# Kernel optimization log

Measured on AMD Instinct MI355X. Metric: run time of the kernel, lower is better.

Reference implementation:

```python
import jax, jax.numpy as jnp
import numpy as np

HEADS = 16


def setup_inputs() -> dict:
    key = jax.random.key(0)
    k1, k2, k3 = jax.random.split(key, 3)
    B, N, C = 4, 2048, 1024
    x = jax.random.normal(k1, (B, N, C), dtype=jnp.float32)
    w_qkv = jax.random.normal(k2, (C, 3 * C), dtype=jnp.float32) * (C ** -0.5)
    b_qkv = jnp.zeros((3 * C,), dtype=jnp.float32)
    w_out = jax.random.normal(k3, (C, C), dtype=jnp.float32) * (C ** -0.5)
    b_out = jnp.zeros((C,), dtype=jnp.float32)
    return {"x": x, "w_qkv": w_qkv, "b_qkv": b_qkv, "w_out": w_out, "b_out": b_out}


def reference(x, w_qkv, b_qkv, w_out, b_out):
    # Dropout layers act as identity in eval mode.
    B, N, C = x.shape
    H = HEADS
    Dh = C // H
    scale = Dh ** -0.5
    qkv = x @ w_qkv + b_qkv                        # [B, N, 3C]
    qkv = qkv.reshape(B, N, 3, H, Dh)
    q = qkv[:, :, 0].transpose(0, 2, 1, 3)         # [B, H, N, Dh]
    k = qkv[:, :, 1].transpose(0, 2, 1, 3)
    v = qkv[:, :, 2].transpose(0, 2, 1, 3)
    attn = jnp.einsum('bhnd,bhmd->bhnm', q, k) * scale
    attn = jax.nn.softmax(attn, axis=-1)
    out = jnp.einsum('bhnm,bhmd->bhnd', attn, v)   # [B, H, N, Dh]
    out = out.transpose(0, 2, 1, 3).reshape(B, N, C)
    return out @ w_out + b_out
```

## Files before the change

kernel.cpp:

```cpp
#include <hip/hip_runtime.h>

typedef __attribute__((ext_vector_type(8))) short bf16x8;
typedef __attribute__((ext_vector_type(4))) float f32x4;
typedef __attribute__((ext_vector_type(16))) float f32x16;

__device__ __forceinline__ ushort f2bf(float f) {
  union { float f; unsigned u; } v; v.f = f;
  unsigned r = v.u + 0x7fffu + ((v.u >> 16) & 1u);
  return (ushort)(r >> 16);
}

__device__ __forceinline__ float bf2f(ushort u) {
  union { float f; unsigned u; } v; v.u = (unsigned)u << 16;
  return v.f;
}

__device__ __forceinline__ unsigned cvt_pk_bf16(float lo, float hi) {
  unsigned r;
  asm("v_cvt_pk_bf16_f32 %0, %1, %2" : "=v"(r) : "v"(lo), "v"(hi));
  return r;
}

__device__ __forceinline__ void permlane32_swap(unsigned& x, unsigned& y) {
  asm("v_permlane32_swap_b32 %0, %1" : "+v"(x), "+v"(y));
}

__device__ __forceinline__ void gload_lds16(const void* g, void* l) {
  __builtin_amdgcn_global_load_lds(
      (const __attribute__((address_space(1))) void*)g,
      (__attribute__((address_space(3))) void*)l, 16, 0, 0);
}


__global__ void cvt_f32_bf16(const float* __restrict__ s, ushort* __restrict__ d, int n) {
  int i = (blockIdx.x * blockDim.x + threadIdx.x) * 4;
  int stride = gridDim.x * blockDim.x * 4;
  for (; i < n; i += stride) {
    float4 v = *reinterpret_cast<const float4*>(s + i);
    ushort4 o;
    o.x = f2bf(v.x); o.y = f2bf(v.y); o.z = f2bf(v.z); o.w = f2bf(v.w);
    *reinterpret_cast<ushort4*>(d + i) = o;
  }
}

__global__ void transpose_cvt(const float* __restrict__ src, ushort* __restrict__ dst,
                              int R, int C) {
  __shared__ float tile[32][33];
  int c0 = blockIdx.x * 32, r0 = blockIdx.y * 32;
  int tx = threadIdx.x, ty = threadIdx.y;
  #pragma unroll
  for (int i = 0; i < 32; i += 8)
    tile[ty + i][tx] = src[(size_t)(r0 + ty + i) * C + c0 + tx];
  __syncthreads();
  #pragma unroll
  for (int i = 0; i < 32; i += 8)
    dst[(size_t)(c0 + ty + i) * R + r0 + tx] = f2bf(tile[tx][ty + i]);
}


#define QK_STAGE(Sp, Gp, base, kt)                                             \
  {                                                                            \
    _Pragma("unroll")                                                          \
    for (int c_ = 0; c_ < 4; ++c_) {                                           \
      const int qq_ = c_ * 512 + tid;                                          \
      const int row_ = qq_ >> 3;                                               \
      const int so_ = ((qq_ & 7) ^ (row_ & 7)) * 8;                            \
      gload_lds16(Gp + (size_t)((base) + row_) * 1024 + (kt) + so_,            \
                  (char*)Sp + qq_ * 16);                                       \
    }                                                                          \
  }

#define QK_LDA(buf, mh)                                                        \
  {                                                                            \
    _Pragma("unroll")                                                          \
    for (int mi = 0; mi < 4; ++mi) {                                           \
      const int row_ = wm * 128 + (mh) * 64 + mi * 16 + lr;                    \
      const char* p_ = (const char*)&sA[buf][0] + row_ * 128;                  \
      const int sw_ = (row_ & 7) << 4;                                         \
      af[mi][0] = *(const bf16x8*)(p_ + ((lg * 16) ^ sw_));                    \
      af[mi][1] = *(const bf16x8*)(p_ + ((64 + lg * 16) ^ sw_));               \
    }                                                                          \
  }

#define QK_LDB(buf, nh)                                                        \
  {                                                                            \
    _Pragma("unroll")                                                          \
    for (int ni = 0; ni < 2; ++ni) {                                           \
      const int row_ = wn * 64 + (nh) * 32 + ni * 16 + lr;                     \
      const char* p_ = (const char*)&sB[buf][0] + row_ * 128;                  \
      const int sw_ = (row_ & 7) << 4;                                         \
      bf[ni][0] = *(const bf16x8*)(p_ + ((lg * 16) ^ sw_));                    \
      bf[ni][1] = *(const bf16x8*)(p_ + ((64 + lg * 16) ^ sw_));               \
    }                                                                          \
  }

#define QK_MMQ(mh, nh)                                                         \
  {                                                                            \
    _Pragma("unroll")                                                          \
    for (int kk = 0; kk < 2; ++kk)                                             \
      _Pragma("unroll")                                                        \
      for (int mi = 0; mi < 4; ++mi)                                           \
        _Pragma("unroll")                                                      \
        for (int ni = 0; ni < 2; ++ni)                                         \
          acc[mh][mi][nh][ni] = __builtin_amdgcn_mfma_f32_16x16x32_bf16(       \
              af[mi][kk], bf[ni][kk], acc[mh][mi][nh][ni], 0, 0, 0);           \
  }

#define QK_SYNC_MMQ(mh, nh)                                                    \
  __builtin_amdgcn_s_barrier();                                                \
  asm volatile("s_waitcnt lgkmcnt(0)" ::: "memory");                           \
  __builtin_amdgcn_sched_barrier(0);                                           \
  __builtin_amdgcn_s_setprio(1);                                               \
  QK_MMQ(mh, nh);                                                              \
  __builtin_amdgcn_s_setprio(0);                                               \
  __builtin_amdgcn_s_barrier();

__global__ __launch_bounds__(512, 1) void gemm_qk(const ushort* __restrict__ A,
                                                  const ushort* __restrict__ Bt,
                                                  const float* __restrict__ bias,
                                                  ushort* __restrict__ q,
                                                  ushort* __restrict__ k) {
  __shared__ __align__(16) ushort sA[2][256 * 64];
  __shared__ __align__(16) ushort sB[2][256 * 64];
  const int tid = threadIdx.x, lane = tid & 63, w = tid >> 6;
  const int wm = w >> 2, wn = w & 3;
  const int lr = lane & 15, lg = lane >> 4;

  const int id = blockIdx.x;
  const int xcd = id & 7, j = id >> 3;
  const int by = xcd * 4 + (j & 3);
  const int bx = j >> 2;
  const int bm = by * 256, bn = bx * 256;

  f32x4 acc[2][4][2][2] = {};
  bf16x8 af[4][2], bf[2][2];

  QK_STAGE(&sA[0][0], A, bm, 0);
  QK_STAGE(&sB[0][0], Bt, bn, 0);
  asm volatile("s_waitcnt vmcnt(0)" ::: "memory");
  __builtin_amdgcn_s_barrier();

  for (int T = 0; T < 16; ++T) {
    const int cur = T & 1;
    const bool pf = (T + 1 < 16);
    QK_LDA(cur, 0); QK_LDB(cur, 0);
    if (pf) QK_STAGE(&sA[cur ^ 1][0], A, bm, (T + 1) * 64);
    QK_SYNC_MMQ(0, 0);
    QK_LDB(cur, 1);
    if (pf) QK_STAGE(&sB[cur ^ 1][0], Bt, bn, (T + 1) * 64);
    QK_SYNC_MMQ(0, 1);
    QK_LDA(cur, 1);
    QK_SYNC_MMQ(1, 1);
    QK_LDB(cur, 0);
    asm volatile("s_waitcnt vmcnt(0)" ::: "memory");
    QK_SYNC_MMQ(1, 0);
  }

  ushort* const dst = (bn < 1024) ? q : k;
  const int cb = bn & 1023;
  #pragma unroll
  for (int mh = 0; mh < 2; ++mh)
    #pragma unroll
    for (int mi = 0; mi < 4; ++mi)
      #pragma unroll
      for (int nh = 0; nh < 2; ++nh)
        #pragma unroll
        for (int ni = 0; ni < 2; ++ni) {
          const int cq = cb + wn * 64 + nh * 32 + ni * 16 + lr;
          const int h = cq >> 6, d = cq & 63;
          const float bb = bias[bn + wn * 64 + nh * 32 + ni * 16 + lr];
          #pragma unroll
          for (int r = 0; r < 4; ++r) {
            const int row = bm + wm * 128 + mh * 64 + mi * 16 + lg * 4 + r;
            const int b_ = row >> 11, n = row & 2047;
            const int bh = b_ * 16 + h;
            dst[((size_t)bh * 2048 + n) * 64 + d] = f2bf(acc[mh][mi][nh][ni][r] + bb);
          }
        }
}


#define GEMM_STAGE(buf, Ap, Bp, kt)                                            \
  {                                                                            \
    _Pragma("unroll")                                                          \
    for (int c_ = 0; c_ < 4; ++c_) {                                           \
      const int qq_ = c_ * 256 + tid;                                          \
      const int row_ = qq_ >> 3;                                               \
      const int so_ = ((qq_ & 7) ^ (row_ & 7)) * 8;                            \
      gload_lds16(Ap + (size_t)(bm + row_) * 1024 + (kt) + so_,                \
                  (char*)sA + (buf) * 16384 + qq_ * 16);                       \
      gload_lds16(Bp + (size_t)(bn + row_) * 1024 + (kt) + so_,                \
                  (char*)sB + (buf) * 16384 + qq_ * 16);                       \
    }                                                                          \
  }

#define GEMM_COMPUTE(buf)                                                      \
  {                                                                            \
    const char* bA_ = (const char*)sA + (buf) * 16384;                         \
    const char* bB_ = (const char*)sB + (buf) * 16384;                         \
    bf16x8 af[4][2], bfr[4][2];                                                \
    _Pragma("unroll")                                                          \
    for (int mi = 0; mi < 4; ++mi) {                                           \
      const int row_ = wr * 64 + mi * 16 + lr;                                 \
      const char* p_ = bA_ + row_ * 128;                                       \
      const int sw_ = (row_ & 7) << 4;                                         \
      af[mi][0] = *(const bf16x8*)(p_ + ((lg * 16) ^ sw_));                    \
      af[mi][1] = *(const bf16x8*)(p_ + ((64 + lg * 16) ^ sw_));               \
    }                                                                          \
    _Pragma("unroll")                                                          \
    for (int ni = 0; ni < 4; ++ni) {                                           \
      const int row_ = wc * 64 + ni * 16 + lr;                                 \
      const char* p_ = bB_ + row_ * 128;                                       \
      const int sw_ = (row_ & 7) << 4;                                         \
      bfr[ni][0] = *(const bf16x8*)(p_ + ((lg * 16) ^ sw_));                   \
      bfr[ni][1] = *(const bf16x8*)(p_ + ((64 + lg * 16) ^ sw_));              \
    }                                                                          \
    _Pragma("unroll")                                                          \
    for (int kk = 0; kk < 2; ++kk)                                             \
      _Pragma("unroll")                                                        \
      for (int mi = 0; mi < 4; ++mi)                                           \
        _Pragma("unroll")                                                      \
        for (int ni = 0; ni < 4; ++ni)                                         \
          acc[mi][ni] = __builtin_amdgcn_mfma_f32_16x16x32_bf16(               \
              af[mi][kk], bfr[ni][kk], acc[mi][ni], 0, 0, 0);                  \
  }

#define GEMM_PIPELINE(Ap, Bp)                                                  \
  GEMM_STAGE(0, Ap, Bp, 0);                                                    \
  for (int T = 0; T < 16; ++T) {                                               \
    if (T + 1 < 16) {                                                          \
      GEMM_STAGE((T + 1) & 1, Ap, Bp, (T + 1) * 64);                           \
      asm volatile("s_waitcnt vmcnt(8)" ::: "memory");                         \
    } else {                                                                   \
      asm volatile("s_waitcnt vmcnt(0)" ::: "memory");                         \
    }                                                                          \
    __builtin_amdgcn_s_barrier();                                              \
    __builtin_amdgcn_sched_barrier(0);                                         \
    GEMM_COMPUTE(T & 1);                                                       \
    __builtin_amdgcn_s_barrier();                                              \
  }

#define GEMM_PROLOG                                                            \
  __shared__ __align__(16) ushort sA[2][128 * 64];                             \
  __shared__ __align__(16) ushort sB[2][128 * 64];                             \
  const int tid = threadIdx.x;                                                 \
  const int lane = tid & 63;                                                   \
  const int w = tid >> 6;                                                      \
  const int wr = w >> 1, wc = w & 1;                                           \
  const int lr = lane & 15, lg = lane >> 4;                                    \
  f32x4 acc[4][4] = {};


__global__ __launch_bounds__(256) void gemm_vT(const ushort* __restrict__ A,
                                               const ushort* __restrict__ Bt,
                                               const float* __restrict__ bias,
                                               ushort* __restrict__ vT) {
  GEMM_PROLOG;
  const int id = blockIdx.x;
  const int xcd = id & 7, j = id >> 3;
  const int bnb = xcd * 8 + (j & 7);
  const int bmb = j >> 3;
  const int bm = bmb * 128;
  const int bn = bnb * 128;

  GEMM_PIPELINE(A, Bt);

  const int b_ = bn >> 11, n0 = bn & 2047;
  #pragma unroll
  for (int mi = 0; mi < 4; ++mi)
    #pragma unroll
    for (int ni = 0; ni < 4; ++ni) {
      const int ncol = wc * 64 + ni * 16 + lr;
      #pragma unroll
      for (int r = 0; r < 4; ++r) {
        const int m = wr * 64 + mi * 16 + lg * 4 + r;
        const int vc = bm + m;
        const int h = vc >> 6, d = vc & 63;
        const int bh = b_ * 16 + h;
        const float bb = bias[vc];
        vT[((size_t)bh * 64 + d) * 2048 + n0 + ncol] = f2bf(acc[mi][ni][r] + bb);
      }
    }
}


__global__ __launch_bounds__(256) void gemm_out(const ushort* __restrict__ A,
                                                const ushort* __restrict__ Bt,
                                                const float* __restrict__ bias,
                                                float* __restrict__ out) {
  GEMM_PROLOG;
  const int id = blockIdx.x;
  const int xcd = id & 7, j = id >> 3;
  const int by = xcd * 8 + (j & 7);
  const int bx = j >> 3;
  const int bm = by * 128;
  const int bn = bx * 128;

  GEMM_PIPELINE(A, Bt);

  #pragma unroll
  for (int mi = 0; mi < 4; ++mi)
    #pragma unroll
    for (int ni = 0; ni < 4; ++ni) {
      const int col = bn + wc * 64 + ni * 16 + lr;
      const float bb = bias[col];
      #pragma unroll
      for (int r = 0; r < 4; ++r) {
        const int row = bm + wr * 64 + mi * 16 + lg * 4 + r;
        out[(size_t)row * 1024 + col] = acc[mi][ni][r] + bb;
      }
    }
}


__global__ __launch_bounds__(512, 2) void attn_fwd(const ushort* __restrict__ q,
                                                   const ushort* __restrict__ k,
                                                   const ushort* __restrict__ vT,
                                                   ushort* __restrict__ o) {
  __shared__ __align__(16) ushort sK[2][64 * 64];
  __shared__ __align__(16) ushort sV[2][64 * 64];

  const int tid = threadIdx.x, lane = tid & 63, w = tid >> 6;
  const int id = blockIdx.x;
  const int xcd = id & 7, j = id >> 3;
  const int bh = xcd * 8 + (j & 7);
  const int qx = j >> 3;
  const int qrow0 = qx * 256 + w * 32;

  const ushort* Qb = q + (size_t)bh * 2048 * 64;
  const ushort* Kb = k + (size_t)bh * 2048 * 64;
  const ushort* Vb = vT + (size_t)bh * 64 * 2048;
  const int lq = lane & 31, hi = lane >> 5;

  const int srow = lane >> 3;
  const int ssw = ((lane & 7) ^ srow) * 8;
  const int krow = w * 8 + srow;

  gload_lds16(Kb + (size_t)krow * 64 + ssw, &sK[0][w * 512]);
  gload_lds16(Vb + (size_t)krow * 2048 + 0 + ssw, &sV[0][w * 512]);

  const float qs = 0.125f * 1.44269504f;
  bf16x8 qf[4];
  #pragma unroll
  for (int dk = 0; dk < 4; ++dk) {
    bf16x8 t = *(const bf16x8*)(Qb + (size_t)(qrow0 + lq) * 64 + dk * 16 + hi * 8);
    #pragma unroll
    for (int jj = 0; jj < 8; ++jj)
      t[jj] = (short)f2bf(bf2f((ushort)t[jj]) * qs);
    qf[dk] = t;
  }

  float m_run = -1e30f, l_run = 0.f;
  f32x16 oacc[2] = {};

  for (int t = 0; t < 32; ++t) {
    const int cur = t & 1;
    if (t + 1 < 32) {
      const int kv2 = (t + 1) << 6;
      gload_lds16(Kb + (size_t)(kv2 + krow) * 64 + ssw, &sK[cur ^ 1][w * 512]);
      gload_lds16(Vb + (size_t)krow * 2048 + kv2 + ssw, &sV[cur ^ 1][w * 512]);
      asm volatile("s_waitcnt vmcnt(2)" ::: "memory");
    } else {
      asm volatile("s_waitcnt vmcnt(0)" ::: "memory");
    }
    __builtin_amdgcn_s_barrier();
    __builtin_amdgcn_sched_barrier(0);

    const char* kb_ = (const char*)&sK[cur][0];
    const char* vb_ = (const char*)&sV[cur][0];

    f32x16 S[2] = {};
    __builtin_amdgcn_s_setprio(1);
    #pragma unroll
    for (int kvt = 0; kvt < 2; ++kvt) {
      const int row = kvt * 32 + lq;
      const int rsw = (row & 7) << 4;
      #pragma unroll
      for (int dk = 0; dk < 4; ++dk) {
        bf16x8 kf = *(const bf16x8*)(kb_ + row * 128 + ((dk * 32 + hi * 16) ^ rsw));
        S[kvt] = __builtin_amdgcn_mfma_f32_32x32x16_bf16(kf, qf[dk], S[kvt], 0, 0, 0);
      }
    }
    __builtin_amdgcn_s_setprio(0);

    float mx = S[0][0];
    #pragma unroll
    for (int kvt = 0; kvt < 2; ++kvt)
      #pragma unroll
      for (int r = 0; r < 16; ++r) mx = fmaxf(mx, S[kvt][r]);
    const float rm = fmaxf(mx, __shfl_xor(mx, 32, 64));

    if (!__all(rm <= m_run + 8.f)) {
      const float mnew = fmaxf(m_run, rm);
      const float corr = __builtin_amdgcn_exp2f(m_run - mnew);
      m_run = mnew;
      l_run *= corr;
      float cq[16];
      #pragma unroll
      for (int r = 0; r < 16; ++r)
        cq[r] = __shfl(corr, (r & 3) + 8 * (r >> 2) + 4 * hi, 64);
      #pragma unroll
      for (int dt = 0; dt < 2; ++dt)
        #pragma unroll
        for (int r = 0; r < 16; ++r) oacc[dt][r] *= cq[r];
    }

    float psum = 0.f;
    unsigned pk_[2][8];
    #pragma unroll
    for (int kvt = 0; kvt < 2; ++kvt) {
      float e[16];
      #pragma unroll
      for (int r = 0; r < 16; ++r) {
        e[r] = __builtin_amdgcn_exp2f(S[kvt][r] - m_run);
        psum += e[r];
      }
      #pragma unroll
      for (int g = 0; g < 4; ++g) {
        pk_[kvt][g * 2 + 0] = cvt_pk_bf16(e[4 * g + 0], e[4 * g + 1]);
        pk_[kvt][g * 2 + 1] = cvt_pk_bf16(e[4 * g + 2], e[4 * g + 3]);
      }
    }
    psum += __shfl_xor(psum, 32, 64);
    l_run += psum;

    __builtin_amdgcn_s_setprio(1);
    #pragma unroll
    for (int kvt = 0; kvt < 2; ++kvt)
      #pragma unroll
      for (int cc = 0; cc < 2; ++cc) {
        unsigned x0 = pk_[kvt][4 * cc + 0], x1 = pk_[kvt][4 * cc + 1];
        unsigned y0 = pk_[kvt][4 * cc + 2], y1 = pk_[kvt][4 * cc + 3];
        permlane32_swap(x0, y0);
        permlane32_swap(x1, y1);
        union { unsigned u[4]; bf16x8 v; } Am;
        Am.u[0] = x0; Am.u[1] = x1; Am.u[2] = y0; Am.u[3] = y1;
        const int cg = kvt * 2 + cc;
        #pragma unroll
        for (int dt = 0; dt < 2; ++dt) {
          const int row = dt * 32 + lq;
          bf16x8 vf = *(const bf16x8*)(vb_ + row * 128 + ((cg * 32 + hi * 16) ^ ((row & 7) << 4)));
          oacc[dt] = __builtin_amdgcn_mfma_f32_32x32x16_bf16(Am.v, vf, oacc[dt], 0, 0, 0);
        }
      }
    __builtin_amdgcn_s_setprio(0);
    __builtin_amdgcn_s_barrier();
  }

  const int b_ = bh >> 4, h = bh & 15;
  float lf[16];
  #pragma unroll
  for (int r = 0; r < 16; ++r)
    lf[r] = __builtin_amdgcn_rcpf(__shfl(l_run, (r & 3) + 8 * (r >> 2) + 4 * hi, 64));
  #pragma unroll
  for (int dt = 0; dt < 2; ++dt)
    #pragma unroll
    for (int r = 0; r < 16; ++r) {
      const int n = qrow0 + (r & 3) + 8 * (r >> 2) + 4 * hi;
      o[(((size_t)b_ * 2048 + n) * 16 + h) * 64 + dt * 32 + lq] = f2bf(oacc[dt][r] * lf[r]);
    }
}


extern "C" void kernel_launch(void* const* d_in, const int* in_sizes, int n_in,
                              void* d_out, int out_size, void* d_ws, size_t ws_size,
                              hipStream_t stream) {
  const float* x = (const float*)d_in[0];
  const float* w_qkv = (const float*)d_in[1];
  const float* b_qkv = (const float*)d_in[2];
  const float* w_out = (const float*)d_in[3];
  const float* b_out = (const float*)d_in[4];
  float* out = (float*)d_out;
  char* ws = (char*)d_ws;

  ushort* xb    = (ushort*)(ws);
  ushort* wqkvT = (ushort*)(ws + 16777216);
  ushort* woutT = (ushort*)(ws + 23068672);
  ushort* qb    = (ushort*)(ws + 25165824);
  ushort* kb    = (ushort*)(ws + 41943040);
  ushort* vTb   = (ushort*)(ws + 58720256);
  ushort* attnb = (ushort*)(ws + 75497472);

  cvt_f32_bf16<<<2048, 256, 0, stream>>>(x, xb, 8192 * 1024);
  transpose_cvt<<<dim3(96, 32), dim3(32, 8), 0, stream>>>(w_qkv, wqkvT, 1024, 3072);
  transpose_cvt<<<dim3(32, 32), dim3(32, 8), 0, stream>>>(w_out, woutT, 1024, 1024);
  gemm_qk<<<256, 512, 0, stream>>>(xb, wqkvT, b_qkv, qb, kb);
  gemm_vT<<<512, 256, 0, stream>>>(wqkvT + 2048 * 1024, xb, b_qkv + 2048, vTb);
  attn_fwd<<<512, 512, 0, stream>>>(qb, kb, vTb, attnb);
  gemm_out<<<512, 256, 0, stream>>>(attnb, woutT, b_out, out);
}
```

Measured before the change: 183.0 us.

## Port gemm_vT and gemm_out to 512-thread 256x128 ping-pong tile pipeline

Rewrites the V-projection and output-projection GEMMs from 128x128 tiles with 256 threads to 256x128 (or 128x256) tiles with 512 threads, reusing the split-stage, barrier-interleaved MFMA pipeline of gemm_qk. Each K step is split into four MFMA quarters, with staged global-to-LDS loads interleaved between them. The goal is more data reuse per block and better overlap of loads with MFMA. The attention kernel's block-to-(bh,qx) mapping is also swapped so all query tiles of a head stay on one XCD. The cost is larger tiles and fewer blocks, 256 instead of 512.

New measurement: 191.4 us. +4.6%, slower.

```diff
diff --git a/kernel.cpp b/kernel.cpp
--- a/kernel.cpp
+++ b/kernel.cpp
@@ -58,40 +58,49 @@
 }
 
 
-#define QK_STAGE(Sp, Gp, base, kt)                                             \
-  {                                                                            \
-    _Pragma("unroll")                                                          \
-    for (int c_ = 0; c_ < 4; ++c_) {                                           \
+#define STAGE_PIECE(Sp, Gp, base, kt, row0)                                    \
+  {                                                                            \
+    _Pragma("unroll")                                                          \
+    for (int c_ = 0; c_ < 2; ++c_) {                                           \
       const int qq_ = c_ * 512 + tid;                                          \
       const int row_ = qq_ >> 3;                                               \
       const int so_ = ((qq_ & 7) ^ (row_ & 7)) * 8;                            \
-      gload_lds16(Gp + (size_t)((base) + row_) * 1024 + (kt) + so_,            \
-                  (char*)Sp + qq_ * 16);                                       \
+      gload_lds16(Gp + (size_t)((base) + (row0) + row_) * 1024 + (kt) + so_,   \
+                  (char*)(Sp) + ((row0) * 8 + qq_) * 16);                      \
     }                                                                          \
   }
 
+#define SYNC_MFMA(BODY)                                                        \
+  __builtin_amdgcn_s_barrier();                                                \
+  asm volatile("s_waitcnt lgkmcnt(0)" ::: "memory");                           \
+  __builtin_amdgcn_sched_barrier(0);                                           \
+  __builtin_amdgcn_s_setprio(1);                                               \
+  BODY;                                                                        \
+  __builtin_amdgcn_s_setprio(0);                                               \
+  __builtin_amdgcn_s_barrier();
+
+#define LDFRAG(dst2, basep, rowexpr)                                           \
+  {                                                                            \
+    const int row_ = (rowexpr);                                                \
+    const char* p_ = (const char*)(basep) + row_ * 128;                        \
+    const int sw_ = (row_ & 7) << 4;                                           \
+    dst2[0] = *(const bf16x8*)(p_ + ((lg * 16) ^ sw_));                        \
+    dst2[1] = *(const bf16x8*)(p_ + ((64 + lg * 16) ^ sw_));                   \
+  }
+
+
 #define QK_LDA(buf, mh)                                                        \
   {                                                                            \
     _Pragma("unroll")                                                          \
-    for (int mi = 0; mi < 4; ++mi) {                                           \
-      const int row_ = wm * 128 + (mh) * 64 + mi * 16 + lr;                    \
-      const char* p_ = (const char*)&sA[buf][0] + row_ * 128;                  \
-      const int sw_ = (row_ & 7) << 4;                                         \
-      af[mi][0] = *(const bf16x8*)(p_ + ((lg * 16) ^ sw_));                    \
-      af[mi][1] = *(const bf16x8*)(p_ + ((64 + lg * 16) ^ sw_));               \
-    }                                                                          \
+    for (int mi = 0; mi < 4; ++mi)                                             \
+      LDFRAG(af[mi], &sA[buf][0], wm * 128 + (mh) * 64 + mi * 16 + lr);        \
   }
 
 #define QK_LDB(buf, nh)                                                        \
   {                                                                            \
     _Pragma("unroll")                                                          \
-    for (int ni = 0; ni < 2; ++ni) {                                           \
-      const int row_ = wn * 64 + (nh) * 32 + ni * 16 + lr;                     \
-      const char* p_ = (const char*)&sB[buf][0] + row_ * 128;                  \
-      const int sw_ = (row_ & 7) << 4;                                         \
-      bf[ni][0] = *(const bf16x8*)(p_ + ((lg * 16) ^ sw_));                    \
-      bf[ni][1] = *(const bf16x8*)(p_ + ((64 + lg * 16) ^ sw_));               \
-    }                                                                          \
+    for (int ni = 0; ni < 2; ++ni)                                             \
+      LDFRAG(bfr[ni], &sB[buf][0], wn * 64 + (nh) * 32 + ni * 16 + lr);        \
   }
 
 #define QK_MMQ(mh, nh)                                                         \
@@ -103,17 +112,8 @@
         _Pragma("unroll")                                                      \
         for (int ni = 0; ni < 2; ++ni)                                         \
           acc[mh][mi][nh][ni] = __builtin_amdgcn_mfma_f32_16x16x32_bf16(       \
-              af[mi][kk], bf[ni][kk], acc[mh][mi][nh][ni], 0, 0, 0);           \
-  }
-
-#define QK_SYNC_MMQ(mh, nh)                                                    \
-  __builtin_amdgcn_s_barrier();                                                \
-  asm volatile("s_waitcnt lgkmcnt(0)" ::: "memory");                           \
-  __builtin_amdgcn_sched_barrier(0);                                           \
-  __builtin_amdgcn_s_setprio(1);                                               \
-  QK_MMQ(mh, nh);                                                              \
-  __builtin_amdgcn_s_setprio(0);                                               \
-  __builtin_amdgcn_s_barrier();
+              af[mi][kk], bfr[ni][kk], acc[mh][mi][nh][ni], 0, 0, 0);          \
+  }
 
 __global__ __launch_bounds__(512, 1) void gemm_qk(const ushort* __restrict__ A,
                                                   const ushort* __restrict__ Bt,
@@ -133,10 +133,10 @@
   const int bm = by * 256, bn = bx * 256;
 
   f32x4 acc[2][4][2][2] = {};
-  bf16x8 af[4][2], bf[2][2];
-
-  QK_STAGE(&sA[0][0], A, bm, 0);
-  QK_STAGE(&sB[0][0], Bt, bn, 0);
+  bf16x8 af[4][2], bfr[2][2];
+
+  STAGE_PIECE(&sA[0][0], A, bm, 0, 0);   STAGE_PIECE(&sA[0][0], A, bm, 0, 128);
+  STAGE_PIECE(&sB[0][0], Bt, bn, 0, 0);  STAGE_PIECE(&sB[0][0], Bt, bn, 0, 128);
   asm volatile("s_waitcnt vmcnt(0)" ::: "memory");
   __builtin_amdgcn_s_barrier();
 
@@ -144,16 +144,18 @@
     const int cur = T & 1;
     const bool pf = (T + 1 < 16);
     QK_LDA(cur, 0); QK_LDB(cur, 0);
-    if (pf) QK_STAGE(&sA[cur ^ 1][0], A, bm, (T + 1) * 64);
-    QK_SYNC_MMQ(0, 0);
+    if (pf) { STAGE_PIECE(&sA[cur ^ 1][0], A, bm, (T + 1) * 64, 0);
+              STAGE_PIECE(&sA[cur ^ 1][0], A, bm, (T + 1) * 64, 128); }
+    SYNC_MFMA(QK_MMQ(0, 0));
     QK_LDB(cur, 1);
-    if (pf) QK_STAGE(&sB[cur ^ 1][0], Bt, bn, (T + 1) * 64);
-    QK_SYNC_MMQ(0, 1);
+    if (pf) { STAGE_PIECE(&sB[cur ^ 1][0], Bt, bn, (T + 1) * 64, 0);
+              STAGE_PIECE(&sB[cur ^ 1][0], Bt, bn, (T + 1) * 64, 128); }
+    SYNC_MFMA(QK_MMQ(0, 1));
     QK_LDA(cur, 1);
-    QK_SYNC_MMQ(1, 1);
+    SYNC_MFMA(QK_MMQ(1, 1));
     QK_LDB(cur, 0);
     asm volatile("s_waitcnt vmcnt(0)" ::: "memory");
-    QK_SYNC_MMQ(1, 0);
+    SYNC_MFMA(QK_MMQ(1, 0));
   }
 
   ushort* const dst = (bn < 1024) ? q : k;
@@ -180,136 +182,169 @@
 }
 
 
-#define GEMM_STAGE(buf, Ap, Bp, kt)                                            \
-  {                                                                            \
-    _Pragma("unroll")                                                          \
-    for (int c_ = 0; c_ < 4; ++c_) {                                           \
-      const int qq_ = c_ * 256 + tid;                                          \
-      const int row_ = qq_ >> 3;                                               \
-      const int so_ = ((qq_ & 7) ^ (row_ & 7)) * 8;                            \
-      gload_lds16(Ap + (size_t)(bm + row_) * 1024 + (kt) + so_,                \
-                  (char*)sA + (buf) * 16384 + qq_ * 16);                       \
-      gload_lds16(Bp + (size_t)(bn + row_) * 1024 + (kt) + so_,                \
-                  (char*)sB + (buf) * 16384 + qq_ * 16);                       \
-    }                                                                          \
-  }
-
-#define GEMM_COMPUTE(buf)                                                      \
-  {                                                                            \
-    const char* bA_ = (const char*)sA + (buf) * 16384;                         \
-    const char* bB_ = (const char*)sB + (buf) * 16384;                         \
-    bf16x8 af[4][2], bfr[4][2];                                                \
-    _Pragma("unroll")                                                          \
-    for (int mi = 0; mi < 4; ++mi) {                                           \
-      const int row_ = wr * 64 + mi * 16 + lr;                                 \
-      const char* p_ = bA_ + row_ * 128;                                       \
-      const int sw_ = (row_ & 7) << 4;                                         \
-      af[mi][0] = *(const bf16x8*)(p_ + ((lg * 16) ^ sw_));                    \
-      af[mi][1] = *(const bf16x8*)(p_ + ((64 + lg * 16) ^ sw_));               \
-    }                                                                          \
-    _Pragma("unroll")                                                          \
-    for (int ni = 0; ni < 4; ++ni) {                                           \
-      const int row_ = wc * 64 + ni * 16 + lr;                                 \
-      const char* p_ = bB_ + row_ * 128;                                       \
-      const int sw_ = (row_ & 7) << 4;                                         \
-      bfr[ni][0] = *(const bf16x8*)(p_ + ((lg * 16) ^ sw_));                   \
-      bfr[ni][1] = *(const bf16x8*)(p_ + ((64 + lg * 16) ^ sw_));              \
-    }                                                                          \
+#define GO_LDA(buf, mh)                                                        \
+  {                                                                            \
+    _Pragma("unroll")                                                          \
+    for (int mi = 0; mi < 4; ++mi)                                             \
+      LDFRAG(af[mi], &sA[buf][0], wm * 128 + (mh) * 64 + mi * 16 + lr);        \
+  }
+
+#define GO_LDB(buf, nh)                                                        \
+  LDFRAG(bfr, &sB[buf][0], wn * 32 + (nh) * 16 + lr);
+
+#define GO_MMQ(mh, nh)                                                         \
+  {                                                                            \
     _Pragma("unroll")                                                          \
     for (int kk = 0; kk < 2; ++kk)                                             \
       _Pragma("unroll")                                                        \
       for (int mi = 0; mi < 4; ++mi)                                           \
-        _Pragma("unroll")                                                      \
-        for (int ni = 0; ni < 4; ++ni)                                         \
-          acc[mi][ni] = __builtin_amdgcn_mfma_f32_16x16x32_bf16(               \
-              af[mi][kk], bfr[ni][kk], acc[mi][ni], 0, 0, 0);                  \
-  }
-
-#define GEMM_PIPELINE(Ap, Bp)                                                  \
-  GEMM_STAGE(0, Ap, Bp, 0);                                                    \
-  for (int T = 0; T < 16; ++T) {                                               \
-    if (T + 1 < 16) {                                                          \
-      GEMM_STAGE((T + 1) & 1, Ap, Bp, (T + 1) * 64);                           \
-      asm volatile("s_waitcnt vmcnt(8)" ::: "memory");                         \
-    } else {                                                                   \
-      asm volatile("s_waitcnt vmcnt(0)" ::: "memory");                         \
-    }                                                                          \
-    __builtin_amdgcn_s_barrier();                                              \
-    __builtin_amdgcn_sched_barrier(0);                                         \
-    GEMM_COMPUTE(T & 1);                                                       \
-    __builtin_amdgcn_s_barrier();                                              \
-  }
-
-#define GEMM_PROLOG                                                            \
-  __shared__ __align__(16) ushort sA[2][128 * 64];                             \
-  __shared__ __align__(16) ushort sB[2][128 * 64];                             \
-  const int tid = threadIdx.x;                                                 \
-  const int lane = tid & 63;                                                   \
-  const int w = tid >> 6;                                                      \
-  const int wr = w >> 1, wc = w & 1;                                           \
-  const int lr = lane & 15, lg = lane >> 4;                                    \
-  f32x4 acc[4][4] = {};
-
-
-__global__ __launch_bounds__(256) void gemm_vT(const ushort* __restrict__ A,
-                                               const ushort* __restrict__ Bt,
-                                               const float* __restrict__ bias,
-                                               ushort* __restrict__ vT) {
-  GEMM_PROLOG;
+        acc[mh][mi][nh] = __builtin_amdgcn_mfma_f32_16x16x32_bf16(             \
+            af[mi][kk], bfr[kk], acc[mh][mi][nh], 0, 0, 0);                    \
+  }
+
+__global__ __launch_bounds__(512, 1) void gemm_out(const ushort* __restrict__ A,
+                                                   const ushort* __restrict__ Bt,
+                                                   const float* __restrict__ bias,
+                                                   float* __restrict__ out) {
+  __shared__ __align__(16) ushort sA[2][256 * 64];
+  __shared__ __align__(16) ushort sB[2][128 * 64];
+  const int tid = threadIdx.x, lane = tid & 63, w = tid >> 6;
+  const int wm = w >> 2, wn = w & 3;
+  const int lr = lane & 15, lg = lane >> 4;
+
   const int id = blockIdx.x;
   const int xcd = id & 7, j = id >> 3;
-  const int bnb = xcd * 8 + (j & 7);
-  const int bmb = j >> 3;
-  const int bm = bmb * 128;
-  const int bn = bnb * 128;
-
-  GEMM_PIPELINE(A, Bt);
-
-  const int b_ = bn >> 11, n0 = bn & 2047;
-  #pragma unroll
-  for (int mi = 0; mi < 4; ++mi)
-    #pragma unroll
-    for (int ni = 0; ni < 4; ++ni) {
-      const int ncol = wc * 64 + ni * 16 + lr;
-      #pragma unroll
-      for (int r = 0; r < 4; ++r) {
-        const int m = wr * 64 + mi * 16 + lg * 4 + r;
-        const int vc = bm + m;
-        const int h = vc >> 6, d = vc & 63;
-        const int bh = b_ * 16 + h;
-        const float bb = bias[vc];
-        vT[((size_t)bh * 64 + d) * 2048 + n0 + ncol] = f2bf(acc[mi][ni][r] + bb);
+  const int by = xcd * 4 + (j & 3);
+  const int bx = j >> 2;
+  const int bm = by * 256, bn = bx * 128;
+
+  f32x4 acc[2][4][2] = {};
+  bf16x8 af[4][2], bfr[2];
+
+  STAGE_PIECE(&sA[0][0], A, bm, 0, 0);  STAGE_PIECE(&sA[0][0], A, bm, 0, 128);
+  STAGE_PIECE(&sB[0][0], Bt, bn, 0, 0);
+  asm volatile("s_waitcnt vmcnt(0)" ::: "memory");
+  __builtin_amdgcn_s_barrier();
+
+  for (int T = 0; T < 16; ++T) {
+    const int cur = T & 1;
+    const bool pf = (T + 1 < 16);
+    GO_LDA(cur, 0); GO_LDB(cur, 0);
+    if (pf) STAGE_PIECE(&sA[cur ^ 1][0], A, bm, (T + 1) * 64, 0);
+    SYNC_MFMA(GO_MMQ(0, 0));
+    GO_LDB(cur, 1);
+    if (pf) STAGE_PIECE(&sA[cur ^ 1][0], A, bm, (T + 1) * 64, 128);
+    SYNC_MFMA(GO_MMQ(0, 1));
+    GO_LDA(cur, 1);
+    if (pf) STAGE_PIECE(&sB[cur ^ 1][0], Bt, bn, (T + 1) * 64, 0);
+    SYNC_MFMA(GO_MMQ(1, 1));
+    GO_LDB(cur, 0);
+    asm volatile("s_waitcnt vmcnt(0)" ::: "memory");
+    SYNC_MFMA(GO_MMQ(1, 0));
+  }
+
+  #pragma unroll
+  for (int mh = 0; mh < 2; ++mh)
+    #pragma unroll
+    for (int mi = 0; mi < 4; ++mi)
+      #pragma unroll
+      for (int nh = 0; nh < 2; ++nh) {
+        const int col = bn + wn * 32 + nh * 16 + lr;
+        const float bb = bias[col];
+        #pragma unroll
+        for (int r = 0; r < 4; ++r) {
+          const int row = bm + wm * 128 + mh * 64 + mi * 16 + lg * 4 + r;
+          out[(size_t)row * 1024 + col] = acc[mh][mi][nh][r] + bb;
+        }
       }
-    }
-}
-
-
-__global__ __launch_bounds__(256) void gemm_out(const ushort* __restrict__ A,
-                                                const ushort* __restrict__ Bt,
-                                                const float* __restrict__ bias,
-                                                float* __restrict__ out) {
-  GEMM_PROLOG;
+}
+
+
+#define GV_LDA(buf, mh)                                                        \
+  {                                                                            \
+    _Pragma("unroll")                                                          \
+    for (int mi = 0; mi < 2; ++mi)                                             \
+      LDFRAG(af[mi], &sA[buf][0], wm * 64 + (mh) * 32 + mi * 16 + lr);         \
+  }
+
+#define GV_LDB(buf, nh)                                                        \
+  {                                                                            \
+    _Pragma("unroll")                                                          \
+    for (int ni = 0; ni < 2; ++ni)                                             \
+      LDFRAG(bfr[ni], &sB[buf][0], wn * 64 + (nh) * 32 + ni * 16 + lr);        \
+  }
+
+#define GV_MMQ(mh, nh)                                                         \
+  {                                                                            \
+    _Pragma("unroll")                                                          \
+    for (int kk = 0; kk < 2; ++kk)                                             \
+      _Pragma("unroll")                                                        \
+      for (int mi = 0; mi < 2; ++mi)                                           \
+        _Pragma("unroll")                                                      \
+        for (int ni = 0; ni < 2; ++ni)                                         \
+          acc[mh][mi][nh][ni] = __builtin_amdgcn_mfma_f32_16x16x32_bf16(       \
+              af[mi][kk], bfr[ni][kk], acc[mh][mi][nh][ni], 0, 0, 0);          \
+  }
+
+__global__ __launch_bounds__(512, 1) void gemm_vT(const ushort* __restrict__ A,
+                                                  const ushort* __restrict__ Bt,
+                                                  const float* __restrict__ bias,
+                                                  ushort* __restrict__ vT) {
+  __shared__ __align__(16) ushort sA[2][128 * 64];
+  __shared__ __align__(16) ushort sB[2][256 * 64];
+  const int tid = threadIdx.x, lane = tid & 63, w = tid >> 6;
+  const int wm = w >> 2, wn = w & 3;
+  const int lr = lane & 15, lg = lane >> 4;
+
   const int id = blockIdx.x;
   const int xcd = id & 7, j = id >> 3;
-  const int by = xcd * 8 + (j & 7);
-  const int bx = j >> 3;
-  const int bm = by * 128;
-  const int bn = bx * 128;
-
-  GEMM_PIPELINE(A, Bt);
-
-  #pragma unroll
-  for (int mi = 0; mi < 4; ++mi)
-    #pragma unroll
-    for (int ni = 0; ni < 4; ++ni) {
-      const int col = bn + wc * 64 + ni * 16 + lr;
-      const float bb = bias[col];
-      #pragma unroll
-      for (int r = 0; r < 4; ++r) {
-        const int row = bm + wr * 64 + mi * 16 + lg * 4 + r;
-        out[(size_t)row * 1024 + col] = acc[mi][ni][r] + bb;
-      }
-    }
+  const int bnb = xcd * 4 + (j & 3);
+  const int bmb = j >> 2;
+  const int bm = bmb * 128, bn = bnb * 256;
+
+  f32x4 acc[2][2][2][2] = {};
+  bf16x8 af[2][2], bfr[2][2];
+
+  STAGE_PIECE(&sB[0][0], Bt, bn, 0, 0);  STAGE_PIECE(&sB[0][0], Bt, bn, 0, 128);
+  STAGE_PIECE(&sA[0][0], A, bm, 0, 0);
+  asm volatile("s_waitcnt vmcnt(0)" ::: "memory");
+  __builtin_amdgcn_s_barrier();
+
+  for (int T = 0; T < 16; ++T) {
+    const int cur = T & 1;
+    const bool pf = (T + 1 < 16);
+    GV_LDA(cur, 0); GV_LDB(cur, 0);
+    if (pf) STAGE_PIECE(&sB[cur ^ 1][0], Bt, bn, (T + 1) * 64, 0);
+    SYNC_MFMA(GV_MMQ(0, 0));
+    GV_LDB(cur, 1);
+    if (pf) STAGE_PIECE(&sB[cur ^ 1][0], Bt, bn, (T + 1) * 64, 128);
+    SYNC_MFMA(GV_MMQ(0, 1));
+    GV_LDA(cur, 1);
+    if (pf) STAGE_PIECE(&sA[cur ^ 1][0], A, bm, (T + 1) * 64, 0);
+    SYNC_MFMA(GV_MMQ(1, 1));
+    GV_LDB(cur, 0);
+    asm volatile("s_waitcnt vmcnt(0)" ::: "memory");
+    SYNC_MFMA(GV_MMQ(1, 0));
+  }
+
+  const int b_ = bn >> 11, n0 = bn & 2047;
+  #pragma unroll
+  for (int mh = 0; mh < 2; ++mh)
+    #pragma unroll
+    for (int mi = 0; mi < 2; ++mi)
+      #pragma unroll
+      for (int nh = 0; nh < 2; ++nh)
+        #pragma unroll
+        for (int ni = 0; ni < 2; ++ni) {
+          const int ncol = wn * 64 + nh * 32 + ni * 16 + lr;
+          #pragma unroll
+          for (int r = 0; r < 4; ++r) {
+            const int vc = bm + wm * 64 + mh * 32 + mi * 16 + lg * 4 + r;
+            const int h = vc >> 6, d = vc & 63;
+            const int bh = b_ * 16 + h;
+            vT[((size_t)bh * 64 + d) * 2048 + n0 + ncol] = f2bf(acc[mh][mi][nh][ni][r] + bias[vc]);
+          }
+        }
 }
 
 
@@ -323,8 +358,8 @@
   const int tid = threadIdx.x, lane = tid & 63, w = tid >> 6;
   const int id = blockIdx.x;
   const int xcd = id & 7, j = id >> 3;
-  const int bh = xcd * 8 + (j & 7);
-  const int qx = j >> 3;
+  const int bh = xcd * 8 + (j >> 3);
+  const int qx = j & 7;
   const int qrow0 = qx * 256 + w * 32;
 
   const ushort* Qb = q + (size_t)bh * 2048 * 64;
@@ -485,7 +520,7 @@
   transpose_cvt<<<dim3(96, 32), dim3(32, 8), 0, stream>>>(w_qkv, wqkvT, 1024, 3072);
   transpose_cvt<<<dim3(32, 32), dim3(32, 8), 0, stream>>>(w_out, woutT, 1024, 1024);
   gemm_qk<<<256, 512, 0, stream>>>(xb, wqkvT, b_qkv, qb, kb);
-  gemm_vT<<<512, 256, 0, stream>>>(wqkvT + 2048 * 1024, xb, b_qkv + 2048, vTb);
+  gemm_vT<<<256, 512, 0, stream>>>(wqkvT + 2048 * 1024, xb, b_qkv + 2048, vTb);
   attn_fwd<<<512, 512, 0, stream>>>(qb, kb, vTb, attnb);
-  gemm_out<<<512, 256, 0, stream>>>(attnb, woutT, b_out, out);
-}
+  gemm_out<<<256, 512, 0, stream>>>(attnb, woutT, b_out, out);
+}
```
